# Performance work log

Hardware: AMD Instinct MI355X
Metric: run time of the kernel (lower is better)

## Reference

```python
import jax, jax.numpy as jnp
import numpy as np

D_MODEL = 512
N_HEADS = 8
MAX_DEPTH = 4
D_FF = 4 * D_MODEL
B, L = 4, 2048


def setup_inputs() -> dict:
    key = jax.random.key(0)
    ks = jax.random.split(key, 16)
    s = 0.02
    inp = {
        "x": jax.random.normal(ks[0], (B, L, D_MODEL), dtype=jnp.float32),
        # attention pre-norm
        "ln1_g": jnp.ones((D_MODEL,), jnp.float32),
        "ln1_b": jnp.zeros((D_MODEL,), jnp.float32),
        # MultiheadAttention in_proj (3D, D) and out_proj (D, D), torch (out, in) layout
        "Wqkv": jax.random.normal(ks[1], (3 * D_MODEL, D_MODEL), jnp.float32) * s,
        "bqkv": jnp.zeros((3 * D_MODEL,), jnp.float32),
        "Wo": jax.random.normal(ks[2], (D_MODEL, D_MODEL), jnp.float32) * s,
        "bo": jnp.zeros((D_MODEL,), jnp.float32),
        # FFN pre-norm + MLP
        "ln2_g": jnp.ones((D_MODEL,), jnp.float32),
        "ln2_b": jnp.zeros((D_MODEL,), jnp.float32),
        "W1": jax.random.normal(ks[3], (D_FF, D_MODEL), jnp.float32) * s,
        "b1": jnp.zeros((D_FF,), jnp.float32),
        "W2": jax.random.normal(ks[4], (D_MODEL, D_FF), jnp.float32) * s,
        "b2": jnp.zeros((D_MODEL,), jnp.float32),
        # token-choice depth router: LayerNorm + Linear(D,D) + GELU + Linear(D,max_depth)
        "rn_g": jnp.ones((D_MODEL,), jnp.float32),
        "rn_b": jnp.zeros((D_MODEL,), jnp.float32),
        "Rw1": jax.random.normal(ks[5], (D_MODEL, D_MODEL), jnp.float32) * s,
        "Rb1": jnp.zeros((D_MODEL,), jnp.float32),
        "Rw2": jax.random.normal(ks[6], (MAX_DEPTH, D_MODEL), jnp.float32) * s,
        "Rb2": jnp.zeros((MAX_DEPTH,), jnp.float32),
    }
    return inp


def _layernorm(x, g, b, eps=1e-5):
    mu = jnp.mean(x, axis=-1, keepdims=True)
    var = jnp.var(x, axis=-1, keepdims=True)
    return (x - mu) * jax.lax.rsqrt(var + eps) * g + b


def _block(x, ln1_g, ln1_b, Wqkv, bqkv, Wo, bo, ln2_g, ln2_b, W1, b1, W2, b2):
    Bb, Ll, D = x.shape
    H = N_HEADS
    dh = D // H
    # pre-norm self-attention
    h = _layernorm(x, ln1_g, ln1_b)
    qkv = h @ Wqkv.T + bqkv                      # (B, L, 3D)
    q, k, v = jnp.split(qkv, 3, axis=-1)
    q = q.reshape(Bb, Ll, H, dh)
    k = k.reshape(Bb, Ll, H, dh)
    v = v.reshape(Bb, Ll, H, dh)
    scores = jnp.einsum("blhd,bmhd->bhlm", q, k) / jnp.sqrt(jnp.float32(dh))
    attn = jax.nn.softmax(scores, axis=-1)
    o = jnp.einsum("bhlm,bmhd->blhd", attn, v).reshape(Bb, Ll, D)
    x = x + (o @ Wo.T + bo)
    # pre-norm FFN (exact-erf GELU, matching torch nn.GELU default)
    h2 = _layernorm(x, ln2_g, ln2_b)
    f = jax.nn.gelu(h2 @ W1.T + b1, approximate=False) @ W2.T + b2
    return x + f


def reference(x, ln1_g, ln1_b, Wqkv, bqkv, Wo, bo, ln2_g, ln2_b, W1, b1, W2, b2,
              rn_g, rn_b, Rw1, Rb1, Rw2, Rb2):
    # --- token-choice depth router (eval mode: argmax) ---
    rh = _layernorm(x, rn_g, rn_b)
    rh = jax.nn.gelu(rh @ Rw1.T + Rb1, approximate=False)
    router_logits = rh @ Rw2.T + Rb2             # (B, L, MAX_DEPTH)
    depths = jnp.argmax(router_logits, axis=-1) + 1  # (B, L) in [1, MAX_DEPTH]
    # --- dense recursion with torch.where-style selection ---
    cur = x
    for level in range(1, MAX_DEPTH + 1):
        upd = _block(cur, ln1_g, ln1_b, Wqkv, bqkv, Wo, bo,
                     ln2_g, ln2_b, W1, b1, W2, b2)
        keep = (depths >= level)[..., None]      # (B, L, 1)
        cur = jnp.where(keep, upd, cur)
    return cur, depths, router_logits
```

## Files before the change

kernel.cpp:

```cpp
#include <hip/hip_runtime.h>

typedef unsigned short u16;
typedef __attribute__((ext_vector_type(8))) short short8;
typedef __attribute__((ext_vector_type(4))) short s16x4;
typedef __attribute__((ext_vector_type(4))) float floatx4;
typedef __attribute__((ext_vector_type(4))) unsigned short u16x4;

#define NTOK 8192
#define DMODEL 512
#define DFF 2048
#define LSEQ 2048

__device__ __forceinline__ u16 f2bf(float f) {
    union { float f; unsigned u; } x; x.f = f;
    unsigned r = (x.u + 0x7fffu + ((x.u >> 16) & 1u)) >> 16;
    return (u16)r;
}

__device__ __forceinline__ float geluf(float x) {
    return 0.5f * x * (1.0f + erff(x * 0.70710678118654752f));
}

__device__ __forceinline__ void gload_lds16(const void* g, void* l) {
    __builtin_amdgcn_global_load_lds(
        (const __attribute__((address_space(1))) void*)g,
        (__attribute__((address_space(3))) void*)l,
        16, 0, 0);
}

__device__ __forceinline__ s16x4 pack_p(float p0, float p1, float p2, float p3) {
    union { float f; unsigned u; } a{p0}, b{p1}, c{p2}, d{p3};
    union { unsigned u[2]; s16x4 s; } r;
    r.u[0] = (a.u >> 16) | (b.u & 0xffff0000u);
    r.u[1] = (c.u >> 16) | (d.u & 0xffff0000u);
    return r.s;
}

__global__ __launch_bounds__(256) void cvt_w(const float* __restrict__ wq,
                                             const float* __restrict__ wo,
                                             const float* __restrict__ w1,
                                             const float* __restrict__ w2,
                                             u16* __restrict__ out) {
    int i = blockIdx.x * 256 + threadIdx.x;
    float v;
    if (i < 786432)       v = wq[i];
    else if (i < 1048576) v = wo[i - 786432];
    else if (i < 2097152) v = w1[i - 1048576];
    else                  v = w2[i - 2097152];
    out[i] = f2bf(v);
}

__global__ __launch_bounds__(256) void copy_f32(const float* __restrict__ a,
                                                float* __restrict__ b) {
    size_t i = ((size_t)blockIdx.x * 256 + threadIdx.x) * 4;
    *(floatx4*)&b[i] = *(const floatx4*)&a[i];
}

template<bool OUTF32>
__global__ __launch_bounds__(256)
void ln_k(const float* __restrict__ x, const float* __restrict__ g,
          const float* __restrict__ bb, void* __restrict__ outp) {
    const int row = blockIdx.x * 4 + (threadIdx.x >> 6);
    const int lane = threadIdx.x & 63;
    const float* xr = x + (size_t)row * DMODEL;
    const int c0 = lane * 4, c1 = c0 + 256;
    floatx4 a = *(const floatx4*)&xr[c0];
    floatx4 b = *(const floatx4*)&xr[c1];
    float s = 0.f, sq = 0.f;
#pragma unroll
    for (int e = 0; e < 4; ++e) { s += a[e]; sq += a[e] * a[e]; }
#pragma unroll
    for (int e = 0; e < 4; ++e) { s += b[e]; sq += b[e] * b[e]; }
#pragma unroll
    for (int m = 32; m >= 1; m >>= 1) {
        s += __shfl_xor(s, m);
        sq += __shfl_xor(sq, m);
    }
    const float mean = s * (1.f / 512.f);
    const float rstd = rsqrtf(sq * (1.f / 512.f) - mean * mean + 1e-5f);
    floatx4 g0 = *(const floatx4*)&g[c0];
    floatx4 g1 = *(const floatx4*)&g[c1];
    floatx4 b0 = *(const floatx4*)&bb[c0];
    floatx4 b1 = *(const floatx4*)&bb[c1];
    floatx4 y0, y1;
#pragma unroll
    for (int e = 0; e < 4; ++e) {
        y0[e] = (a[e] - mean) * rstd * g0[e] + b0[e];
        y1[e] = (b[e] - mean) * rstd * g1[e] + b1[e];
    }
    if (OUTF32) {
        float* o = (float*)outp + (size_t)row * DMODEL;
        *(floatx4*)&o[c0] = y0;
        *(floatx4*)&o[c1] = y1;
    } else {
        u16* o = (u16*)outp + (size_t)row * DMODEL;
        u16x4 p0, p1;
#pragma unroll
        for (int e = 0; e < 4; ++e) { p0[e] = f2bf(y0[e]); p1[e] = f2bf(y1[e]); }
        *(u16x4*)&o[c0] = p0;
        *(u16x4*)&o[c1] = p1;
    }
}

template<int EPI, int BN>
__global__ __launch_bounds__(256, 2)
void gemm_bt(const u16* __restrict__ A, const u16* __restrict__ Bw,
             const float* __restrict__ bias,
             u16* __restrict__ Cb, float* __restrict__ Cf,
             const float* __restrict__ res, const float* __restrict__ depth,
             u16* __restrict__ Cv,
             float aux, int N, int K) {
    constexpr int NJ = BN / 32;
    __shared__ __align__(16) u16 As[128 * 32];
    __shared__ __align__(16) u16 Bs[BN * 32];
    const int tid = threadIdx.x;
    const int lane = tid & 63;
    const int w = tid >> 6;
    const int wm = (w >> 1) * 64;
    const int wn = (w & 1) * (BN / 2);
    const int mBase = blockIdx.x * 128;
    const int nBase = blockIdx.y * BN;
    const int q4 = lane >> 4, rl = lane & 15;

    floatx4 acc[4][NJ];
#pragma unroll
    for (int i = 0; i < 4; ++i)
#pragma unroll
        for (int j = 0; j < NJ; ++j) acc[i][j] = (floatx4){0.f, 0.f, 0.f, 0.f};

    const int i0 = tid, i1 = tid + 256;
    const int ar0 = i0 >> 2, ac0 = ((i0 & 3) ^ ((i0 >> 3) & 3)) * 8;
    const int ar1 = i1 >> 2, ac1 = ((i1 & 3) ^ ((i1 >> 3) & 3)) * 8;
    const u16* pA0 = A + (size_t)(mBase + ar0) * K + ac0;
    const u16* pA1 = A + (size_t)(mBase + ar1) * K + ac1;
    const u16* pB0 = Bw + (size_t)(nBase + ar0) * K + ac0;
    const u16* pB1 = (BN == 128) ? Bw + (size_t)(nBase + ar1) * K + ac1 : pB0;
    u16* lA0 = &As[i0 * 8];
    u16* lA1 = &As[i1 * 8];
    u16* lB0 = &Bs[i0 * 8];
    u16* lB1 = (BN == 128) ? &Bs[i1 * 8] : lB0;

    for (int k0 = 0; k0 < K; k0 += 32) {
        gload_lds16(pA0, lA0);
        gload_lds16(pA1, lA1);
        gload_lds16(pB0, lB0);
        if (BN == 128) gload_lds16(pB1, lB1);
        pA0 += 32; pA1 += 32; pB0 += 32;
        if (BN == 128) pB1 += 32;
        __syncthreads();
        short8 af[4], bf[NJ];
#pragma unroll
        for (int t = 0; t < 4; ++t) {
            const int r = wm + t * 16 + rl;
            af[t] = *(const short8*)&As[r * 32 + (q4 ^ ((r >> 1) & 3)) * 8];
        }
#pragma unroll
        for (int t = 0; t < NJ; ++t) {
            const int r = wn + t * 16 + rl;
            bf[t] = *(const short8*)&Bs[r * 32 + (q4 ^ ((r >> 1) & 3)) * 8];
        }
#pragma unroll
        for (int ti = 0; ti < 4; ++ti)
#pragma unroll
            for (int tj = 0; tj < NJ; ++tj)
                acc[ti][tj] = __builtin_amdgcn_mfma_f32_16x16x32_bf16(
                    af[ti], bf[tj], acc[ti][tj], 0, 0, 0);
        __syncthreads();
    }

#pragma unroll
    for (int ti = 0; ti < 4; ++ti) {
        const int r0 = mBase + wm + ti * 16 + q4 * 4;
#pragma unroll
        for (int tj = 0; tj < NJ; ++tj) {
            const int c = nBase + wn + tj * 16 + rl;
            const float bv = bias[c];
            if (EPI == 0) {
                if (nBase < 1024) {
                    const float sc = (nBase < 512) ? aux : 1.0f;
#pragma unroll
                    for (int rr = 0; rr < 4; ++rr)
                        Cb[(size_t)(r0 + rr) * 1024 + c] =
                            f2bf((acc[ti][tj][rr] + bv) * sc);
                } else {
                    const int cm = c - 1024;
                    const int hh = cm >> 6, dh = cm & 63;
                    const int bb2 = r0 >> 11, kv = r0 & 2047;
                    u16x4 pk;
#pragma unroll
                    for (int rr = 0; rr < 4; ++rr)
                        pk[rr] = f2bf(acc[ti][tj][rr] + bv);
                    *(u16x4*)&Cv[((size_t)(bb2 * 8 + hh) * 64 + dh) * 2048 + kv] = pk;
                }
            } else {
#pragma unroll
                for (int rr = 0; rr < 4; ++rr) {
                    const int r = r0 + rr;
                    const float v = acc[ti][tj][rr] + bv;
                    if (EPI == 1) {
                        Cb[(size_t)r * N + c] = f2bf(geluf(v));
                    } else if (EPI == 2) {
                        Cf[(size_t)r * N + c] = res[(size_t)r * N + c] + v;
                    } else {
                        if (depth[r] >= aux)
                            Cf[(size_t)r * N + c] = res[(size_t)r * N + c] + v;
                    }
                }
            }
        }
    }
}

__global__ __launch_bounds__(256, 4)
void attn_k(const u16* __restrict__ qk, const u16* __restrict__ vT,
            u16* __restrict__ o) {
    const int qt = blockIdx.x;
    const int bh = blockIdx.y;
    const int b = bh >> 3, h = bh & 7;
    const int tid = threadIdx.x, lane = tid & 63, w = tid >> 6;
    const int tok0 = b * LSEQ;
    const int qrow0 = qt * 64 + w * 16;
    const int q4 = lane >> 4, rl = lane & 15;

    __shared__ __align__(16) u16 Kt[128 * 64];
    __shared__ __align__(16) u16 Vt[64 * 128];

    const u16* vbase = vT + (size_t)bh * 64 * 2048;

    short8 qf[2];
#pragma unroll
    for (int ks = 0; ks < 2; ++ks)
        qf[ks] = *(const short8*)&qk[(size_t)(tok0 + qrow0 + rl) * 1024
                                      + h * 64 + ks * 32 + q4 * 8];

    floatx4 oacc[4];
#pragma unroll
    for (int dt = 0; dt < 4; ++dt) oacc[dt] = (floatx4){0.f, 0.f, 0.f, 0.f};
    float lsum = 0.f;

    for (int kt = 0; kt < 16; ++kt) {
        const int kv0 = kt * 128;
        __syncthreads();
#pragma unroll
        for (int it = 0; it < 4; ++it) {
            const int i = it * 256 + tid;
            const int r = i >> 3;
            const int c = ((i & 7) ^ (r & 7)) * 8;
            gload_lds16(&qk[(size_t)(tok0 + kv0 + r) * 1024 + 512 + h * 64 + c],
                        &Kt[i * 8]);
        }
#pragma unroll
        for (int it = 0; it < 4; ++it) {
            const int i = it * 256 + tid;
            const int dh = i >> 4;
            const int ch = (i & 15) ^ (dh & 15);
            gload_lds16(&vbase[(size_t)dh * 2048 + kv0 + ch * 8], &Vt[i * 8]);
        }
        __syncthreads();

#pragma unroll
        for (int mt = 0; mt < 8; ++mt) {
            const int r = mt * 16 + rl;
            short8 kf0 = *(const short8*)&Kt[r * 64 + ((q4) ^ (r & 7)) * 8];
            short8 kf1 = *(const short8*)&Kt[r * 64 + ((4 + q4) ^ (r & 7)) * 8];
            floatx4 s;
            s = __builtin_amdgcn_mfma_f32_16x16x32_bf16(kf0, qf[0],
                    (floatx4){0.f, 0.f, 0.f, 0.f}, 0, 0, 0);
            s = __builtin_amdgcn_mfma_f32_16x16x32_bf16(kf1, qf[1], s, 0, 0, 0);
            const float p0 = exp2f(s[0]);
            const float p1 = exp2f(s[1]);
            const float p2 = exp2f(s[2]);
            const float p3 = exp2f(s[3]);
            lsum += (p0 + p1) + (p2 + p3);
            const s16x4 pb = pack_p(p0, p1, p2, p3);
            const int ct = 2 * mt + (q4 >> 1);
#pragma unroll
            for (int dt = 0; dt < 4; ++dt) {
                const s16x4 vf = *(const s16x4*)&Vt[(dt * 16 + rl) * 128
                                                    + (ct ^ rl) * 8 + (q4 & 1) * 4];
                oacc[dt] = __builtin_amdgcn_mfma_f32_16x16x16bf16_1k(
                    vf, pb, oacc[dt], 0, 0, 0);
            }
        }
    }

    float l = lsum;
    l += __shfl_xor(l, 16);
    l += __shfl_xor(l, 32);
    const float inv = 1.0f / l;
    const size_t row = tok0 + qrow0 + rl;
#pragma unroll
    for (int dt = 0; dt < 4; ++dt) {
        u16x4 pk;
#pragma unroll
        for (int rr = 0; rr < 4; ++rr) pk[rr] = f2bf(oacc[dt][rr] * inv);
        *(u16x4*)&o[row * DMODEL + h * 64 + dt * 16 + q4 * 4] = pk;
    }
}

__global__ __launch_bounds__(256, 2)
void router_gemm1(const float* __restrict__ A, const float* __restrict__ W,
                  const float* __restrict__ bias, float* __restrict__ out) {
    __shared__ float Af[32][68];
    __shared__ float Bf[32][132];
    const int tid = threadIdx.x;
    const int tx = tid & 15, ty = tid >> 4;
    const int mb = blockIdx.x * 64, nb = blockIdx.y * 128;
    double acc[4][8] = {};
    for (int k0 = 0; k0 < 512; k0 += 32) {
#pragma unroll
        for (int it = 0; it < 2; ++it) {
            const int ch = tid + it * 256;
            const int m = ch >> 3, c4 = (ch & 7) * 4;
            const floatx4 v = *(const floatx4*)&A[(size_t)(mb + m) * 512 + k0 + c4];
#pragma unroll
            for (int e = 0; e < 4; ++e) Af[c4 + e][m] = v[e];
        }
#pragma unroll
        for (int it = 0; it < 4; ++it) {
            const int ch = tid + it * 256;
            const int n = ch >> 3, c4 = (ch & 7) * 4;
            const floatx4 v = *(const floatx4*)&W[(size_t)(nb + n) * 512 + k0 + c4];
#pragma unroll
            for (int e = 0; e < 4; ++e) Bf[c4 + e][n] = v[e];
        }
        __syncthreads();
#pragma unroll 4
        for (int kk = 0; kk < 32; ++kk) {
            const floatx4 a4 = *(const floatx4*)&Af[kk][ty * 4];
            double av[4], bv[8];
#pragma unroll
            for (int i = 0; i < 4; ++i) av[i] = (double)a4[i];
#pragma unroll
            for (int j = 0; j < 8; ++j) bv[j] = (double)Bf[kk][tx + 16 * j];
#pragma unroll
            for (int i = 0; i < 4; ++i)
#pragma unroll
                for (int j = 0; j < 8; ++j)
                    acc[i][j] = fma(av[i], bv[j], acc[i][j]);
        }
        __syncthreads();
    }
#pragma unroll
    for (int i = 0; i < 4; ++i) {
        const int r = mb + ty * 4 + i;
#pragma unroll
        for (int j = 0; j < 8; ++j) {
            const int c = nb + tx + 16 * j;
            out[(size_t)r * 512 + c] = geluf((float)(acc[i][j] + (double)bias[c]));
        }
    }
}

__global__ __launch_bounds__(256)
void router_logits_k(const float* __restrict__ rr, const float* __restrict__ Rw2,
                     const float* __restrict__ Rb2, float* __restrict__ logits,
                     float* __restrict__ depthf) {
    const int t = blockIdx.x * 4 + (threadIdx.x >> 6);
    const int lane = threadIdx.x & 63;
    const float* xr = rr + (size_t)t * 512;
    const int c0 = lane * 4, c1 = c0 + 256;
    floatx4 a = *(const floatx4*)&xr[c0];
    floatx4 b = *(const floatx4*)&xr[c1];
    double s[4];
#pragma unroll
    for (int d = 0; d < 4; ++d) {
        const float* wr = Rw2 + d * 512;
        floatx4 wa = *(const floatx4*)&wr[c0];
        floatx4 wb = *(const floatx4*)&wr[c1];
        double acc = 0.0;
#pragma unroll
        for (int e = 0; e < 4; ++e) acc += (double)a[e] * (double)wa[e];
#pragma unroll
        for (int e = 0; e < 4; ++e) acc += (double)b[e] * (double)wb[e];
        s[d] = acc;
    }
#pragma unroll
    for (int m = 32; m >= 1; m >>= 1)
#pragma unroll
        for (int d = 0; d < 4; ++d) s[d] += __shfl_xor(s[d], m);
    if (lane == 0) {
        double bv = -1e300;
        int best = 0;
#pragma unroll
        for (int d = 0; d < 4; ++d) {
            const double v = s[d] + (double)Rb2[d];
            logits[(size_t)t * 4 + d] = (float)v;
            if (v > bv) { bv = v; best = d; }
        }
        depthf[t] = (float)(best + 1);
    }
}

extern "C" void kernel_launch(void* const* d_in, const int* in_sizes, int n_in,
                              void* d_out, int out_size, void* d_ws, size_t ws_size,
                              hipStream_t stream) {
    (void)in_sizes; (void)n_in; (void)out_size; (void)ws_size;
    const float* x    = (const float*)d_in[0];
    const float* ln1g = (const float*)d_in[1];
    const float* ln1b = (const float*)d_in[2];
    const float* Wqkv = (const float*)d_in[3];
    const float* bqkv = (const float*)d_in[4];
    const float* Wo   = (const float*)d_in[5];
    const float* bo   = (const float*)d_in[6];
    const float* ln2g = (const float*)d_in[7];
    const float* ln2b = (const float*)d_in[8];
    const float* W1   = (const float*)d_in[9];
    const float* b1   = (const float*)d_in[10];
    const float* W2   = (const float*)d_in[11];
    const float* b2   = (const float*)d_in[12];
    const float* rng  = (const float*)d_in[13];
    const float* rnb  = (const float*)d_in[14];
    const float* Rw1  = (const float*)d_in[15];
    const float* Rb1  = (const float*)d_in[16];
    const float* Rw2  = (const float*)d_in[17];
    const float* Rb2  = (const float*)d_in[18];

    float* cur    = (float*)d_out;
    float* depthf = cur + (size_t)NTOK * DMODEL;
    float* logits = depthf + NTOK;

    char* ws = (char*)d_ws;
    float* xmid = (float*)ws;
    u16* sbuf   = (u16*)(ws + 16777216);
    u16* qk     = (u16*)(ws + 25165824);
    u16* ffb    = (u16*)(ws + 41943040);
    u16* vTb    = (u16*)(ws + 75497472);
    u16* wbf    = (u16*)(ws + 83886080);
    float* rrf  = (float*)ffb;

    u16* wq = wbf;
    u16* wo = wbf + 786432;
    u16* w1 = wbf + 1048576;
    u16* w2 = wbf + 2097152;

    const float qsc = 0.125f * 1.4426950408889634f;

    cvt_w<<<12288, 256, 0, stream>>>(Wqkv, Wo, W1, W2, wbf);
    copy_f32<<<4096, 256, 0, stream>>>(x, cur);

    ln_k<true><<<2048, 256, 0, stream>>>(x, rng, rnb, xmid);
    router_gemm1<<<dim3(128, 4), 256, 0, stream>>>(xmid, Rw1, Rb1, rrf);
    router_logits_k<<<2048, 256, 0, stream>>>(rrf, Rw2, Rb2, logits, depthf);

    for (int level = 1; level <= 4; ++level) {
        ln_k<false><<<2048, 256, 0, stream>>>(cur, ln1g, ln1b, sbuf);
        gemm_bt<0, 128><<<dim3(64, 12), 256, 0, stream>>>(
            sbuf, wq, bqkv, qk, nullptr, nullptr, nullptr, vTb, qsc, 1536, 512);
        attn_k<<<dim3(32, 32), 256, 0, stream>>>(qk, vTb, sbuf);
        gemm_bt<2, 64><<<dim3(64, 8), 256, 0, stream>>>(
            sbuf, wo, bo, nullptr, xmid, cur, nullptr, nullptr, 0.f, 512, 512);
        ln_k<false><<<2048, 256, 0, stream>>>(xmid, ln2g, ln2b, sbuf);
        gemm_bt<1, 128><<<dim3(64, 16), 256, 0, stream>>>(
            sbuf, w1, b1, ffb, nullptr, nullptr, nullptr, nullptr, 0.f, 2048, 512);
        gemm_bt<3, 64><<<dim3(64, 8), 256, 0, stream>>>(
            ffb, w2, b2, nullptr, cur, xmid, depthf, nullptr, (float)level, 512, 2048);
    }
}
```

Before: 941.0 us.

## Replace FP64 router GEMM with split-bf16 MFMA plus exact fallback for close tokens

The double-precision router first-layer GEMM is replaced by a bf16 matrix-core GEMM on hi/lo split operands (hi*hi + lo*hi + hi*lo concatenated along K), followed by an fp32 logits kernel. Tokens whose top two logits fall within a small margin are put on a list via an atomic counter and recomputed in FP64 by a fallback kernel, so the argmax depth stays stable. This removes the slow FP64 FMA throughput cost and adds extra conversion kernels, a longer-K GEMM, and a data-dependent fallback pass. Correctness depends on the margin being wide enough to cover the split-bf16 error.

```diff
diff --git a/kernel.cpp b/kernel.cpp
--- a/kernel.cpp
+++ b/kernel.cpp
@@ -10,11 +10,16 @@
 #define DMODEL 512
 #define DFF 2048
 #define LSEQ 2048
+#define RMARGIN 1e-3f
 
 __device__ __forceinline__ u16 f2bf(float f) {
     union { float f; unsigned u; } x; x.f = f;
     unsigned r = (x.u + 0x7fffu + ((x.u >> 16) & 1u)) >> 16;
     return (u16)r;
+}
+__device__ __forceinline__ float bf2f(u16 h) {
+    union { unsigned u; float f; } x; x.u = ((unsigned)h) << 16;
+    return x.f;
 }
 
 __device__ __forceinline__ float geluf(float x) {
@@ -54,6 +59,38 @@
                                                 float* __restrict__ b) {
     size_t i = ((size_t)blockIdx.x * 256 + threadIdx.x) * 4;
     *(floatx4*)&b[i] = *(const floatx4*)&a[i];
+}
+
+__global__ __launch_bounds__(256) void cvt_rw1(const float* __restrict__ Rw1,
+                                               u16* __restrict__ out) {
+    const int i = blockIdx.x * 256 + threadIdx.x;
+    const int n = i >> 9, k = i & 511;
+    const float v = Rw1[i];
+    const u16 hi = f2bf(v);
+    const u16 lo = f2bf(v - bf2f(hi));
+    out[(size_t)n * 1536 + k] = hi;
+    out[(size_t)n * 1536 + 512 + k] = hi;
+    out[(size_t)n * 1536 + 1024 + k] = lo;
+}
+
+__global__ __launch_bounds__(256) void cvt_split(const float* __restrict__ x,
+                                                 u16* __restrict__ out,
+                                                 int* __restrict__ cnt) {
+    if (blockIdx.x == 0 && threadIdx.x == 0) *cnt = 0;
+    const int i = blockIdx.x * 256 + threadIdx.x;
+    const int base = i * 4;
+    const int row = base >> 9, k = base & 511;
+    const floatx4 v = *(const floatx4*)&x[base];
+    u16x4 h, l;
+#pragma unroll
+    for (int e = 0; e < 4; ++e) {
+        h[e] = f2bf(v[e]);
+        l[e] = f2bf(v[e] - bf2f(h[e]));
+    }
+    u16* o = out + (size_t)row * 1536;
+    *(u16x4*)&o[k] = h;
+    *(u16x4*)&o[512 + k] = l;
+    *(u16x4*)&o[1024 + k] = h;
 }
 
 template<bool OUTF32>
@@ -201,9 +238,11 @@
                         Cb[(size_t)r * N + c] = f2bf(geluf(v));
                     } else if (EPI == 2) {
                         Cf[(size_t)r * N + c] = res[(size_t)r * N + c] + v;
-                    } else {
+                    } else if (EPI == 3) {
                         if (depth[r] >= aux)
                             Cf[(size_t)r * N + c] = res[(size_t)r * N + c] + v;
+                    } else {
+                        Cf[(size_t)r * N + c] = geluf(v);
                     }
                 }
             }
@@ -298,81 +337,28 @@
     }
 }
 
-__global__ __launch_bounds__(256, 2)
-void router_gemm1(const float* __restrict__ A, const float* __restrict__ W,
-                  const float* __restrict__ bias, float* __restrict__ out) {
-    __shared__ float Af[32][68];
-    __shared__ float Bf[32][132];
-    const int tid = threadIdx.x;
-    const int tx = tid & 15, ty = tid >> 4;
-    const int mb = blockIdx.x * 64, nb = blockIdx.y * 128;
-    double acc[4][8] = {};
-    for (int k0 = 0; k0 < 512; k0 += 32) {
-#pragma unroll
-        for (int it = 0; it < 2; ++it) {
-            const int ch = tid + it * 256;
-            const int m = ch >> 3, c4 = (ch & 7) * 4;
-            const floatx4 v = *(const floatx4*)&A[(size_t)(mb + m) * 512 + k0 + c4];
-#pragma unroll
-            for (int e = 0; e < 4; ++e) Af[c4 + e][m] = v[e];
-        }
-#pragma unroll
-        for (int it = 0; it < 4; ++it) {
-            const int ch = tid + it * 256;
-            const int n = ch >> 3, c4 = (ch & 7) * 4;
-            const floatx4 v = *(const floatx4*)&W[(size_t)(nb + n) * 512 + k0 + c4];
-#pragma unroll
-            for (int e = 0; e < 4; ++e) Bf[c4 + e][n] = v[e];
-        }
-        __syncthreads();
-#pragma unroll 4
-        for (int kk = 0; kk < 32; ++kk) {
-            const floatx4 a4 = *(const floatx4*)&Af[kk][ty * 4];
-            double av[4], bv[8];
-#pragma unroll
-            for (int i = 0; i < 4; ++i) av[i] = (double)a4[i];
-#pragma unroll
-            for (int j = 0; j < 8; ++j) bv[j] = (double)Bf[kk][tx + 16 * j];
-#pragma unroll
-            for (int i = 0; i < 4; ++i)
-#pragma unroll
-                for (int j = 0; j < 8; ++j)
-                    acc[i][j] = fma(av[i], bv[j], acc[i][j]);
-        }
-        __syncthreads();
-    }
-#pragma unroll
-    for (int i = 0; i < 4; ++i) {
-        const int r = mb + ty * 4 + i;
-#pragma unroll
-        for (int j = 0; j < 8; ++j) {
-            const int c = nb + tx + 16 * j;
-            out[(size_t)r * 512 + c] = geluf((float)(acc[i][j] + (double)bias[c]));
-        }
-    }
-}
-
 __global__ __launch_bounds__(256)
-void router_logits_k(const float* __restrict__ rr, const float* __restrict__ Rw2,
-                     const float* __restrict__ Rb2, float* __restrict__ logits,
-                     float* __restrict__ depthf) {
+void router_logits_f32(const float* __restrict__ rr, const float* __restrict__ Rw2,
+                       const float* __restrict__ Rb2, float* __restrict__ logits,
+                       float* __restrict__ depthf, int* __restrict__ cnt,
+                       int* __restrict__ list) {
     const int t = blockIdx.x * 4 + (threadIdx.x >> 6);
     const int lane = threadIdx.x & 63;
     const float* xr = rr + (size_t)t * 512;
     const int c0 = lane * 4, c1 = c0 + 256;
     floatx4 a = *(const floatx4*)&xr[c0];
     floatx4 b = *(const floatx4*)&xr[c1];
-    double s[4];
+    float s[4];
 #pragma unroll
     for (int d = 0; d < 4; ++d) {
         const float* wr = Rw2 + d * 512;
         floatx4 wa = *(const floatx4*)&wr[c0];
         floatx4 wb = *(const floatx4*)&wr[c1];
-        double acc = 0.0;
-#pragma unroll
-        for (int e = 0; e < 4; ++e) acc += (double)a[e] * (double)wa[e];
-#pragma unroll
-        for (int e = 0; e < 4; ++e) acc += (double)b[e] * (double)wb[e];
+        float acc = 0.f;
+#pragma unroll
+        for (int e = 0; e < 4; ++e) acc += a[e] * wa[e];
+#pragma unroll
+        for (int e = 0; e < 4; ++e) acc += b[e] * wb[e];
         s[d] = acc;
     }
 #pragma unroll
@@ -380,15 +366,71 @@
 #pragma unroll
         for (int d = 0; d < 4; ++d) s[d] += __shfl_xor(s[d], m);
     if (lane == 0) {
-        double bv = -1e300;
-        int best = 0;
+        float v[4];
+        float bv = -1e30f; int best = 0;
 #pragma unroll
         for (int d = 0; d < 4; ++d) {
-            const double v = s[d] + (double)Rb2[d];
-            logits[(size_t)t * 4 + d] = (float)v;
-            if (v > bv) { bv = v; best = d; }
-        }
+            v[d] = s[d] + Rb2[d];
+            logits[(size_t)t * 4 + d] = v[d];
+            if (v[d] > bv) { bv = v[d]; best = d; }
+        }
+        float second = -1e30f;
+#pragma unroll
+        for (int d = 0; d < 4; ++d)
+            if (d != best) second = fmaxf(second, v[d]);
         depthf[t] = (float)(best + 1);
+        if (bv - second < RMARGIN) {
+            int idx = atomicAdd(cnt, 1);
+            list[idx] = t;
+        }
+    }
+}
+
+__global__ __launch_bounds__(256)
+void router_exact(const float* __restrict__ rh, const float* __restrict__ Rw1,
+                  const float* __restrict__ Rb1, const float* __restrict__ Rw2,
+                  const float* __restrict__ Rb2, const int* __restrict__ cnt,
+                  const int* __restrict__ list, float* __restrict__ logits,
+                  float* __restrict__ depthf) {
+    __shared__ float rhs[512];
+    __shared__ double rrd[512];
+    __shared__ double lg[4];
+    const int n = *cnt;
+    const int tid = threadIdx.x;
+    for (int ii = blockIdx.x; ii < n; ii += gridDim.x) {
+        const int t = list[ii];
+        rhs[tid] = rh[(size_t)t * 512 + tid];
+        rhs[tid + 256] = rh[(size_t)t * 512 + 256 + tid];
+        __syncthreads();
+#pragma unroll
+        for (int oo = 0; oo < 2; ++oo) {
+            const int nn = tid + oo * 256;
+            double acc = (double)Rb1[nn];
+            const float* wrow = Rw1 + (size_t)nn * 512;
+            for (int k = 0; k < 512; ++k)
+                acc = fma((double)rhs[k], (double)wrow[k], acc);
+            rrd[nn] = 0.5 * acc * (1.0 + erf(acc * 0.70710678118654752440));
+        }
+        __syncthreads();
+        const int w = tid >> 6, lane = tid & 63;
+        double acc2 = 0.0;
+        for (int k = lane; k < 512; k += 64)
+            acc2 += rrd[k] * (double)Rw2[w * 512 + k];
+#pragma unroll
+        for (int m = 32; m >= 1; m >>= 1) acc2 += __shfl_xor(acc2, m);
+        if (lane == 0) lg[w] = acc2 + (double)Rb2[w];
+        __syncthreads();
+        if (tid == 0) {
+            double bv = -1e300; int best = 0;
+#pragma unroll
+            for (int d = 0; d < 4; ++d) {
+                const double v = lg[d];
+                logits[(size_t)t * 4 + d] = (float)v;
+                if (v > bv) { bv = v; best = d; }
+            }
+            depthf[t] = (float)(best + 1);
+        }
+        __syncthreads();
     }
 }
 
@@ -427,7 +469,12 @@
     u16* ffb    = (u16*)(ws + 41943040);
     u16* vTb    = (u16*)(ws + 75497472);
     u16* wbf    = (u16*)(ws + 83886080);
-    float* rrf  = (float*)ffb;
+
+    u16* rw1s   = (u16*)(ws + 16777216);
+    int* rcnt   = (int*)(ws + 18874368);
+    int* rlist  = rcnt + 16;
+    u16* asplit = ffb;
+    float* rrf  = (float*)qk;
 
     u16* wq = wbf;
     u16* wo = wbf + 786432;
@@ -440,8 +487,14 @@
     copy_f32<<<4096, 256, 0, stream>>>(x, cur);
 
     ln_k<true><<<2048, 256, 0, stream>>>(x, rng, rnb, xmid);
-    router_gemm1<<<dim3(128, 4), 256, 0, stream>>>(xmid, Rw1, Rb1, rrf);
-    router_logits_k<<<2048, 256, 0, stream>>>(rrf, Rw2, Rb2, logits, depthf);
+    cvt_rw1<<<1024, 256, 0, stream>>>(Rw1, rw1s);
+    cvt_split<<<4096, 256, 0, stream>>>(xmid, asplit, rcnt);
+    gemm_bt<4, 64><<<dim3(64, 8), 256, 0, stream>>>(
+        asplit, rw1s, Rb1, nullptr, rrf, nullptr, nullptr, nullptr, 0.f, 512, 1536);
+    router_logits_f32<<<2048, 256, 0, stream>>>(rrf, Rw2, Rb2, logits, depthf,
+                                                rcnt, rlist);
+    router_exact<<<128, 256, 0, stream>>>(xmid, Rw1, Rb1, Rw2, Rb2, rcnt, rlist,
+                                          logits, depthf);
 
     for (int level = 1; level <= 4; ++level) {
         ln_k<false><<<2048, 256, 0, stream>>>(cur, ln1g, ln1b, sbuf);
```

Result: faster. 907.6 us (-3.5%).
